# Optimization experiments

Hardware: AMD Instinct MI355X
Metric: run time of the kernel (lower is better)

The kernel has to match this reference:

```python
import jax, jax.numpy as jnp
import numpy as np

Q_MIN = 0.01
PT_THLD = 0.9
MAX_ETA = 4.0
LW_REP = 1.0
LW_NOISE = 0.1
LW_COWARD = 0.1
EPS = 1e-9

N_HITS = 50000
N_CLUSTERS = 1024  # cluster id 0 = noise, ids 1..K-1 = objects
D_EMB = 32


def setup_inputs() -> dict:
    key = jax.random.key(0)
    k0, k1, k2, k3, k4, k5 = jax.random.split(key, 6)
    beta = jax.random.uniform(k0, (N_HITS,), dtype=jnp.float32)
    x = jax.random.normal(k1, (N_HITS, D_EMB), dtype=jnp.float32)
    pt = jax.random.uniform(k2, (N_HITS,), dtype=jnp.float32)
    eta = jax.random.normal(k3, (N_HITS,), dtype=jnp.float32)
    reconstructable = jax.random.randint(k4, (N_HITS,), 0, 2, dtype=jnp.int32)
    cluster_ids = jax.random.randint(k5, (N_HITS,), 0, N_CLUSTERS, dtype=jnp.int64)
    return {
        'beta': beta, 'x': x, 'pt': pt, 'eta': eta,
        'reconstructable': reconstructable, 'cluster_ids': cluster_ids,
        'n_clusters': N_CLUSTERS,
    }


def reference(beta, x, pt, eta, reconstructable, cluster_ids, n_clusters):
    K = int(n_clusters)
    n_hits = beta.shape[0]
    n_part = K - 1  # objects of interest (excluding noise id 0)

    # charge q_j = arctanh(beta)^2 + q_min
    q = jnp.arctanh(jnp.clip(beta, 0.0, 1.0 - 1e-4)) ** 2 + Q_MIN  # [N]

    # attractive membership mask [N, K-1]: hit j belongs to object k and passes filters
    oids = jnp.arange(1, K)
    hit_ok = (reconstructable > 0) & (pt > PT_THLD) & (jnp.abs(eta) < MAX_ETA)
    att = (cluster_ids[:, None] == oids[None, :]) & hit_ok[:, None]
    attf = att.astype(q.dtype)

    # condensation point per object: hit with max charge within the object
    alphas = jnp.argmax(q[:, None] * attf, axis=0)  # [K-1]
    q_k = q[alphas]
    x_k = x[alphas]  # [K-1, D]

    # pairwise Euclidean distances, GEMM form (avoids [N,K,D] intermediate)
    d2 = (jnp.sum(x * x, axis=1)[:, None]
          + jnp.sum(x_k * x_k, axis=1)[None, :]
          - 2.0 * (x @ x_k.T))
    dist = jnp.sqrt(jnp.maximum(d2, 1e-12))  # [N, K-1]

    qw = q[:, None] * q_k[None, :]

    n_hits_oi = jnp.sum(hit_ok).astype(q.dtype)
    norm_att = EPS + n_hits_oi - n_part
    norm_rep = EPS + (n_part - 1) * n_hits

    v_att = jnp.sum(qw * (dist ** 2) * attf) / norm_att

    rep = (~att) & (dist < 1.0)  # max_n_rep=0 -> no subsampling
    v_rep = jnp.sum(qw * (1.0 - dist) * rep.astype(q.dtype)) / norm_rep

    l_coward = jnp.mean(1.0 - beta[alphas])

    noise_mask = (cluster_ids <= 0).astype(q.dtype)  # noise_threshold = 0
    l_noise = jnp.sum(beta * noise_mask) / jnp.maximum(jnp.sum(noise_mask), 1.0)

    total = v_att + LW_REP * v_rep + LW_NOISE * l_noise + LW_COWARD * l_coward
    return total
```

## Files before the change

### kernel.cpp

```cpp
#include <hip/hip_runtime.h>
#include <math.h>

namespace {

constexpr int D = 32;
constexpr int KOBJ = 1023;
constexpr float QMIN = 0.01f;
constexpr float PTT = 0.9f;
constexpr float METAETA = 4.0f;

typedef __attribute__((ext_vector_type(8))) short short8;
typedef __attribute__((ext_vector_type(4))) float f32x4;

#define GLOAD_LDS16(g, l)                                              \
  __builtin_amdgcn_global_load_lds(                                    \
      (const __attribute__((address_space(1))) void*)(g),              \
      (__attribute__((address_space(3))) void*)(l), 16, 0, 0)

__device__ inline float waveSum(float v) {
#pragma unroll
  for (int o = 32; o > 0; o >>= 1) v += __shfl_down(v, o, 64);
  return v;
}

__device__ inline ushort f2bf(float f) {
  unsigned u = __float_as_uint(f);
  return (ushort)((u + 0x7FFFu + ((u >> 16) & 1u)) >> 16);
}


__global__ __launch_bounds__(256) void k_hits(
    const float* __restrict__ beta, const float* __restrict__ x,
    const float* __restrict__ pt, const float* __restrict__ eta,
    const int* __restrict__ recon, const int* __restrict__ cidw,
    int N, float* acc, unsigned long long* keys,
    float* __restrict__ qArr, float* __restrict__ nxArr,
    int* __restrict__ attkArr) {
  int t = threadIdx.x;
  int j = blockIdx.x * 256 + t;
  int odd = 2 * (t & 127) + 1;
  int ow = (odd < N) ? cidw[odd] : 0;
  int is64 = !__any(ow != 0);
  bool ok = false;
  if (j < N) {
    int cid = is64 ? cidw[2 * j] : cidw[j];
    float b = beta[j];
    float bc = fminf(fmaxf(b, 0.f), 1.f - 1e-4f);
    float tt = atanhf(bc);
    float q = tt * tt + QMIN;
    ok = (recon[j] > 0) && (pt[j] > PTT) && (fabsf(eta[j]) < METAETA);
    float nx = 0.f;
    const float4* xr = (const float4*)(x + (size_t)j * D);
#pragma unroll
    for (int i2 = 0; i2 < 8; ++i2) {
      float4 v = xr[i2];
      nx += v.x * v.x + v.y * v.y + v.z * v.z + v.w * v.w;
    }
    int attk = (ok && cid >= 1) ? cid : 0;
    qArr[j] = q;
    nxArr[j] = nx;
    attkArr[j] = attk;
    if (cid <= 0) {
      atomicAdd(&acc[2], b);
      atomicAdd(&acc[3], 1.f);
    }
    if (attk >= 1) {
      unsigned long long key =
          (((unsigned long long)__float_as_uint(q)) << 32) |
          (unsigned long long)(0xFFFFFFFFu - (unsigned)j);
      atomicMax(&keys[attk - 1], key);
    }
  }
  unsigned long long bal = __ballot(ok);
  if ((t & 63) == 0 && bal)
    atomicAdd(&acc[4], (float)__popcll(bal));
}

__global__ __launch_bounds__(256, 2) void k_clusters(
    const float* __restrict__ beta, const float* __restrict__ x,
    const unsigned long long* __restrict__ keys,
    const float* __restrict__ qArr, const float* __restrict__ nxArr,
    int* __restrict__ alphaArr, float2* __restrict__ qnk,
    ushort* __restrict__ xkbT, float* acc) {
  int k = blockIdx.x * blockDim.x + threadIdx.x;
  float cw = 0.f;
  if (k < KOBJ) {
    unsigned long long key = keys[k];
    int alpha = (key != 0ull) ? (int)(0xFFFFFFFFu - (unsigned)(key & 0xFFFFFFFFull)) : 0;
    alphaArr[k] = alpha;
    qnk[k] = make_float2(qArr[alpha], nxArr[alpha]);
    const float4* s4 = (const float4*)(x + (size_t)alpha * D);
    float4 v[8];
#pragma unroll
    for (int i = 0; i < 8; ++i) v[i] = s4[i];
#pragma unroll
    for (int s = 0; s < 4; ++s) {
      float4 v0 = v[2 * s], v1 = v[2 * s + 1];
      ushort* dst = xkbT + (size_t)s * 8192 + (size_t)k * 8;
      dst[0] = f2bf(v0.x); dst[1] = f2bf(v0.y);
      dst[2] = f2bf(v0.z); dst[3] = f2bf(v0.w);
      dst[4] = f2bf(v1.x); dst[5] = f2bf(v1.y);
      dst[6] = f2bf(v1.z); dst[7] = f2bf(v1.w);
    }
    cw = 1.f - beta[alpha];
  } else if (k == KOBJ) {
    qnk[k] = make_float2(0.f, 1e30f);
#pragma unroll
    for (int s = 0; s < 4; ++s) {
      ushort* dst = xkbT + (size_t)s * 8192 + (size_t)k * 8;
#pragma unroll
      for (int e = 0; e < 8; ++e) dst[e] = 0;
    }
  }
  float s = waveSum(cw);
  if ((threadIdx.x & 63) == 0 && s != 0.f) atomicAdd(&acc[5], s);
}

__global__ __launch_bounds__(256) void k_pair(
    const float* __restrict__ x, int N,
    const float* __restrict__ qArr, const float* __restrict__ nxArr,
    const int* __restrict__ attkArr, const int* __restrict__ alphaArr,
    const float2* __restrict__ qnk, const ushort* __restrict__ xkbT,
    float* acc) {
  __shared__ char lds[16384 + 2048 + 64];
  float* redS = (float*)(lds + 18432);
  int t = threadIdx.x;
  int wv = t >> 6;
  int ln = t & 63;
  int ot = blockIdx.y;
  int ob = ot * 256;
  int rowbase = blockIdx.x * 128;

  for (int c = wv; c < 18; c += 4) {
    const char* src;
    if (c < 16)
      src = (const char*)xkbT + (c >> 2) * 16384 + ob * 16 + (c & 3) * 1024;
    else
      src = (const char*)qnk + ob * 8 + (c - 16) * 1024;
    GLOAD_LDS16(src + ln * 16, lds + c * 1024);
  }

  int lr = ln & 15;
  int lk = ln >> 4;
  int wrow = rowbase + wv * 32;

  short8 am2[2];
#pragma unroll
  for (int rt = 0; rt < 2; ++rt) {
    int row = min(wrow + rt * 16 + lr, N - 1);
    const float* p = x + (size_t)row * D + lk * 8;
    float4 v0 = *(const float4*)p;
    float4 v1 = *(const float4*)(p + 4);
    short8 a;
    a[0] = (short)f2bf(-2.f * v0.x); a[1] = (short)f2bf(-2.f * v0.y);
    a[2] = (short)f2bf(-2.f * v0.z); a[3] = (short)f2bf(-2.f * v0.w);
    a[4] = (short)f2bf(-2.f * v1.x); a[5] = (short)f2bf(-2.f * v1.y);
    a[6] = (short)f2bf(-2.f * v1.z); a[7] = (short)f2bf(-2.f * v1.w);
    am2[rt] = a;
  }
  float nxr[2][4], qrow[2][4];
#pragma unroll
  for (int rt = 0; rt < 2; ++rt)
#pragma unroll
    for (int i = 0; i < 4; ++i) {
      int row = wrow + rt * 16 + lk * 4 + i;
      int rc = min(row, N - 1);
      nxr[rt][i] = (row < N) ? nxArr[rc] : 1e37f;
      qrow[rt][i] = (row < N) ? qArr[rc] : 0.f;
    }
  __syncthreads();

  const float2* qnkS = (const float2*)(lds + 16384);
  float rep = 0.f;
#pragma unroll 4
  for (int tt = 0; tt < 16; ++tt) {
    int o = tt * 16 + lr;
    short8 b = *(const short8*)(lds + lk * 4096 + o * 16);
    float2 qn = qnkS[o];
    float nk = qn.y;
    f32x4 c0 = {nxr[0][0] + nk, nxr[0][1] + nk, nxr[0][2] + nk, nxr[0][3] + nk};
    f32x4 c1 = {nxr[1][0] + nk, nxr[1][1] + nk, nxr[1][2] + nk, nxr[1][3] + nk};
    f32x4 s0 = __builtin_amdgcn_mfma_f32_16x16x32_bf16(am2[0], b, c0, 0, 0, 0);
    f32x4 s1 = __builtin_amdgcn_mfma_f32_16x16x32_bf16(am2[1], b, c1, 0, 0, 0);
    float m = fminf(fminf(fminf(s0[0], s0[1]), fminf(s0[2], s0[3])),
                    fminf(fminf(s1[0], s1[1]), fminf(s1[2], s1[3])));
    if (__any(m < 1.f)) {
      float qk = qn.x;
#pragma unroll
      for (int i = 0; i < 4; ++i) {
        if (s0[i] < 1.f)
          rep += qrow[0][i] * qk * (1.f - sqrtf(fmaxf(s0[i], 1e-12f)));
        if (s1[i] < 1.f)
          rep += qrow[1][i] * qk * (1.f - sqrtf(fmaxf(s1[i], 1e-12f)));
      }
    }
  }

  float attc = 0.f, repSub = 0.f;
  if (ot == 0) {
    int j = rowbase + (t >> 1);
    int qt = t & 1;
    if (j < N) {
      int attk = attkArr[j];
      if (attk >= 1) {
        int k0 = attk - 1;
        int alpha = alphaArr[k0];
        float2 qn = qnk[k0];
        const float4* xj = (const float4*)(x + (size_t)j * D + qt * 16);
        const float4* xk = (const float4*)(x + (size_t)alpha * D + qt * 16);
        float dot = 0.f;
#pragma unroll
        for (int i = 0; i < 4; ++i) {
          float4 a = xj[i], bb = xk[i];
          dot += a.x * bb.x + a.y * bb.y + a.z * bb.z + a.w * bb.w;
        }
        dot += __shfl_xor(dot, 1, 2);
        if (qt == 0) {
          float d2 = nxArr[j] + qn.y - 2.f * dot;
          float w = qArr[j] * qn.x;
          attc = w * fmaxf(d2, 1e-12f);
          if (d2 < 1.f)
            repSub = w * (1.f - sqrtf(fmaxf(d2, 1e-12f)));
        }
      }
    }
  }

  float sw = waveSum(rep);
  float sa = waveSum(attc);
  float sr = waveSum(repSub);
  if (ln == 0) {
    redS[wv] = sw;
    redS[4 + wv] = sa;
    redS[8 + wv] = sr;
  }
  __syncthreads();
  if (t == 0) {
    float tot = (redS[0] + redS[1]) + (redS[2] + redS[3]);
    float ta = (redS[4] + redS[5]) + (redS[6] + redS[7]);
    float tr = (redS[8] + redS[9]) + (redS[10] + redS[11]);
    if (tot != tr) atomicAdd(&acc[1], tot - tr);
    if (ta != 0.f) atomicAdd(&acc[0], ta);
  }
}

__global__ void k_final(const float* __restrict__ acc, int N, float* out) {
  if (threadIdx.x == 0 && blockIdx.x == 0) {
    double attSum = acc[0], repSum = acc[1], noiseSum = acc[2];
    double noiseCnt = acc[3], okCnt = acc[4], cowardSum = acc[5];
    double norm_att = 1e-9 + okCnt - (double)KOBJ;
    double norm_rep = 1e-9 + (double)(KOBJ - 1) * (double)N;
    double v_att = attSum / norm_att;
    double v_rep = repSum / norm_rep;
    double l_coward = cowardSum / (double)KOBJ;
    double l_noise = noiseSum / fmax(noiseCnt, 1.0);
    out[0] = (float)(v_att + 1.0 * v_rep + 0.1 * l_noise + 0.1 * l_coward);
  }
}

}

extern "C" void kernel_launch(void* const* d_in, const int* in_sizes, int n_in,
                              void* d_out, int out_size, void* d_ws, size_t ws_size,
                              hipStream_t stream) {
  const float* beta = (const float*)d_in[0];
  const float* x = (const float*)d_in[1];
  const float* pt = (const float*)d_in[2];
  const float* eta = (const float*)d_in[3];
  const int* recon = (const int*)d_in[4];
  const int* cidw = (const int*)d_in[5];
  int N = in_sizes[0];
  float* out = (float*)d_out;

  char* w = (char*)d_ws;
  float* acc = (float*)w;
  unsigned long long* keys = (unsigned long long*)(w + 64);
  int* alphaArr = (int*)(w + 8256);
  float2* qnk = (float2*)(w + 12352);
  ushort* xkbT = (ushort*)(w + 20544);
  float* qArr = (float*)(w + 86080);
  float* nxArr = (float*)(w + 86080 + (size_t)N * 4);
  int* attkArr = (int*)(w + 86080 + (size_t)N * 8);

  int nbN = (N + 255) / 256;
  int rowgroups = (N + 127) / 128;

  hipMemsetAsync(w, 0, 8256, stream);
  k_hits<<<nbN, 256, 0, stream>>>(beta, x, pt, eta, recon, cidw, N,
                                  acc, keys, qArr, nxArr, attkArr);
  k_clusters<<<4, 256, 0, stream>>>(beta, x, keys, qArr, nxArr,
                                    alphaArr, qnk, xkbT, acc);
  dim3 gp(rowgroups, 4);
  k_pair<<<gp, 256, 0, stream>>>(x, N, qArr, nxArr, attkArr,
                                 alphaArr, qnk, xkbT, acc);
  k_final<<<1, 64, 0, stream>>>(acc, N, out);
}
```

Baseline: 53.58 us.

## Fuse cluster prep and final reduction into pair kernel, cut launches and atomics

```diff
diff --git a/kernel.cpp b/kernel.cpp
--- a/kernel.cpp
+++ b/kernel.cpp
@@ -12,11 +12,6 @@
 typedef __attribute__((ext_vector_type(8))) short short8;
 typedef __attribute__((ext_vector_type(4))) float f32x4;
 
-#define GLOAD_LDS16(g, l)                                              \
-  __builtin_amdgcn_global_load_lds(                                    \
-      (const __attribute__((address_space(1))) void*)(g),              \
-      (__attribute__((address_space(3))) void*)(l), 16, 0, 0)
-
 __device__ inline float waveSum(float v) {
 #pragma unroll
   for (int o = 32; o > 0; o >>= 1) v += __shfl_down(v, o, 64);
@@ -28,6 +23,13 @@
   return (ushort)((u + 0x7FFFu + ((u >> 16) & 1u)) >> 16);
 }
 
+__device__ inline int keyAlpha(unsigned long long key) {
+  return (key != 0ull) ? (int)(0xFFFFFFFFu - (unsigned)(key & 0xFFFFFFFFull)) : 0;
+}
+
+__global__ void k_init(int* wsbase) {
+  for (int k = threadIdx.x; k < 2064; k += 256) wsbase[k] = 0;
+}
 
 __global__ __launch_bounds__(256) void k_hits(
     const float* __restrict__ beta, const float* __restrict__ x,
@@ -42,6 +44,7 @@
   int ow = (odd < N) ? cidw[odd] : 0;
   int is64 = !__any(ow != 0);
   bool ok = false;
+  float nsum = 0.f, ncnt = 0.f;
   if (j < N) {
     int cid = is64 ? cidw[2 * j] : cidw[j];
     float b = beta[j];
@@ -60,10 +63,7 @@
     qArr[j] = q;
     nxArr[j] = nx;
     attkArr[j] = attk;
-    if (cid <= 0) {
-      atomicAdd(&acc[2], b);
-      atomicAdd(&acc[3], 1.f);
-    }
+    if (cid <= 0) { nsum = b; ncnt = 1.f; }
     if (attk >= 1) {
       unsigned long long key =
           (((unsigned long long)__float_as_uint(q)) << 32) |
@@ -71,59 +71,23 @@
       atomicMax(&keys[attk - 1], key);
     }
   }
+  float ws2 = waveSum(nsum);
+  float ws3 = waveSum(ncnt);
   unsigned long long bal = __ballot(ok);
-  if ((t & 63) == 0 && bal)
-    atomicAdd(&acc[4], (float)__popcll(bal));
-}
-
-__global__ __launch_bounds__(256, 2) void k_clusters(
-    const float* __restrict__ beta, const float* __restrict__ x,
-    const unsigned long long* __restrict__ keys,
+  if ((t & 63) == 0) {
+    if (ws3 != 0.f) { atomicAdd(&acc[2], ws2); atomicAdd(&acc[3], ws3); }
+    if (bal) atomicAdd(&acc[4], (float)__popcll(bal));
+  }
+}
+
+__global__ __launch_bounds__(256) void k_pair_all(
+    const float* __restrict__ beta, const float* __restrict__ x, int N,
     const float* __restrict__ qArr, const float* __restrict__ nxArr,
-    int* __restrict__ alphaArr, float2* __restrict__ qnk,
-    ushort* __restrict__ xkbT, float* acc) {
-  int k = blockIdx.x * blockDim.x + threadIdx.x;
-  float cw = 0.f;
-  if (k < KOBJ) {
-    unsigned long long key = keys[k];
-    int alpha = (key != 0ull) ? (int)(0xFFFFFFFFu - (unsigned)(key & 0xFFFFFFFFull)) : 0;
-    alphaArr[k] = alpha;
-    qnk[k] = make_float2(qArr[alpha], nxArr[alpha]);
-    const float4* s4 = (const float4*)(x + (size_t)alpha * D);
-    float4 v[8];
-#pragma unroll
-    for (int i = 0; i < 8; ++i) v[i] = s4[i];
-#pragma unroll
-    for (int s = 0; s < 4; ++s) {
-      float4 v0 = v[2 * s], v1 = v[2 * s + 1];
-      ushort* dst = xkbT + (size_t)s * 8192 + (size_t)k * 8;
-      dst[0] = f2bf(v0.x); dst[1] = f2bf(v0.y);
-      dst[2] = f2bf(v0.z); dst[3] = f2bf(v0.w);
-      dst[4] = f2bf(v1.x); dst[5] = f2bf(v1.y);
-      dst[6] = f2bf(v1.z); dst[7] = f2bf(v1.w);
-    }
-    cw = 1.f - beta[alpha];
-  } else if (k == KOBJ) {
-    qnk[k] = make_float2(0.f, 1e30f);
-#pragma unroll
-    for (int s = 0; s < 4; ++s) {
-      ushort* dst = xkbT + (size_t)s * 8192 + (size_t)k * 8;
-#pragma unroll
-      for (int e = 0; e < 8; ++e) dst[e] = 0;
-    }
-  }
-  float s = waveSum(cw);
-  if ((threadIdx.x & 63) == 0 && s != 0.f) atomicAdd(&acc[5], s);
-}
-
-__global__ __launch_bounds__(256) void k_pair(
-    const float* __restrict__ x, int N,
-    const float* __restrict__ qArr, const float* __restrict__ nxArr,
-    const int* __restrict__ attkArr, const int* __restrict__ alphaArr,
-    const float2* __restrict__ qnk, const ushort* __restrict__ xkbT,
-    float* acc) {
+    const int* __restrict__ attkArr, const unsigned long long* __restrict__ keys,
+    float* acc, unsigned* ticket, float* out) {
   __shared__ char lds[16384 + 2048 + 64];
   float* redS = (float*)(lds + 18432);
+  float2* qnkS = (float2*)(lds + 16384);
   int t = threadIdx.x;
   int wv = t >> 6;
   int ln = t & 63;
@@ -131,13 +95,39 @@
   int ob = ot * 256;
   int rowbase = blockIdx.x * 128;
 
-  for (int c = wv; c < 18; c += 4) {
-    const char* src;
-    if (c < 16)
-      src = (const char*)xkbT + (c >> 2) * 16384 + ob * 16 + (c & 3) * 1024;
-    else
-      src = (const char*)qnk + ob * 8 + (c - 16) * 1024;
-    GLOAD_LDS16(src + ln * 16, lds + c * 1024);
+  {
+    int o = ob + t;
+    float qk = 0.f, nk = 1e30f;
+    if (o < KOBJ) {
+      int alpha = keyAlpha(keys[o]);
+      qk = qArr[alpha];
+      nk = nxArr[alpha];
+      const float4* s4 = (const float4*)(x + (size_t)alpha * D);
+      float4 v[8];
+#pragma unroll
+      for (int i = 0; i < 8; ++i) v[i] = s4[i];
+#pragma unroll
+      for (int s = 0; s < 4; ++s) {
+        float4 v0 = v[2 * s], v1 = v[2 * s + 1];
+        short8 a;
+        a[0] = (short)f2bf(v0.x); a[1] = (short)f2bf(v0.y);
+        a[2] = (short)f2bf(v0.z); a[3] = (short)f2bf(v0.w);
+        a[4] = (short)f2bf(v1.x); a[5] = (short)f2bf(v1.y);
+        a[6] = (short)f2bf(v1.z); a[7] = (short)f2bf(v1.w);
+        *(short8*)(lds + s * 4096 + t * 16) = a;
+      }
+    } else {
+      short8 z = {0, 0, 0, 0, 0, 0, 0, 0};
+#pragma unroll
+      for (int s = 0; s < 4; ++s) *(short8*)(lds + s * 4096 + t * 16) = z;
+    }
+    qnkS[t] = make_float2(qk, nk);
+  }
+
+  float cw = 0.f;
+  if (blockIdx.x == 0) {
+    int o = ob + t;
+    if (o < KOBJ) cw = 1.f - beta[keyAlpha(keys[o])];
   }
 
   int lr = ln & 15;
@@ -170,7 +160,6 @@
     }
   __syncthreads();
 
-  const float2* qnkS = (const float2*)(lds + 16384);
   float rep = 0.f;
 #pragma unroll 4
   for (int tt = 0; tt < 16; ++tt) {
@@ -203,9 +192,7 @@
     if (j < N) {
       int attk = attkArr[j];
       if (attk >= 1) {
-        int k0 = attk - 1;
-        int alpha = alphaArr[k0];
-        float2 qn = qnk[k0];
+        int alpha = keyAlpha(keys[attk - 1]);
         const float4* xj = (const float4*)(x + (size_t)j * D + qt * 16);
         const float4* xk = (const float4*)(x + (size_t)alpha * D + qt * 16);
         float dot = 0.f;
@@ -216,8 +203,8 @@
         }
         dot += __shfl_xor(dot, 1, 2);
         if (qt == 0) {
-          float d2 = nxArr[j] + qn.y - 2.f * dot;
-          float w = qArr[j] * qn.x;
+          float d2 = nxArr[j] + nxArr[alpha] - 2.f * dot;
+          float w = qArr[j] * qArr[alpha];
           attc = w * fmaxf(d2, 1e-12f);
           if (d2 < 1.f)
             repSub = w * (1.f - sqrtf(fmaxf(d2, 1e-12f)));
@@ -229,32 +216,38 @@
   float sw = waveSum(rep);
   float sa = waveSum(attc);
   float sr = waveSum(repSub);
+  float sc = waveSum(cw);
   if (ln == 0) {
-    redS[wv] = sw;
-    redS[4 + wv] = sa;
-    redS[8 + wv] = sr;
+    redS[wv] = sw; redS[4 + wv] = sa; redS[8 + wv] = sr; redS[12 + wv] = sc;
   }
   __syncthreads();
   if (t == 0) {
     float tot = (redS[0] + redS[1]) + (redS[2] + redS[3]);
     float ta = (redS[4] + redS[5]) + (redS[6] + redS[7]);
     float tr = (redS[8] + redS[9]) + (redS[10] + redS[11]);
+    float tc = (redS[12] + redS[13]) + (redS[14] + redS[15]);
     if (tot != tr) atomicAdd(&acc[1], tot - tr);
     if (ta != 0.f) atomicAdd(&acc[0], ta);
-  }
-}
-
-__global__ void k_final(const float* __restrict__ acc, int N, float* out) {
-  if (threadIdx.x == 0 && blockIdx.x == 0) {
-    double attSum = acc[0], repSum = acc[1], noiseSum = acc[2];
-    double noiseCnt = acc[3], okCnt = acc[4], cowardSum = acc[5];
-    double norm_att = 1e-9 + okCnt - (double)KOBJ;
-    double norm_rep = 1e-9 + (double)(KOBJ - 1) * (double)N;
-    double v_att = attSum / norm_att;
-    double v_rep = repSum / norm_rep;
-    double l_coward = cowardSum / (double)KOBJ;
-    double l_noise = noiseSum / fmax(noiseCnt, 1.0);
-    out[0] = (float)(v_att + 1.0 * v_rep + 0.1 * l_noise + 0.1 * l_coward);
+    if (tc != 0.f) atomicAdd(&acc[5], tc);
+
+    unsigned total = gridDim.x * gridDim.y;
+    unsigned old = __hip_atomic_fetch_add(ticket, 1u, __ATOMIC_ACQ_REL,
+                                          __HIP_MEMORY_SCOPE_AGENT);
+    if (old == total - 1) {
+      double attSum = __hip_atomic_load(&acc[0], __ATOMIC_RELAXED, __HIP_MEMORY_SCOPE_AGENT);
+      double repSum = __hip_atomic_load(&acc[1], __ATOMIC_RELAXED, __HIP_MEMORY_SCOPE_AGENT);
+      double noiseSum = __hip_atomic_load(&acc[2], __ATOMIC_RELAXED, __HIP_MEMORY_SCOPE_AGENT);
+      double noiseCnt = __hip_atomic_load(&acc[3], __ATOMIC_RELAXED, __HIP_MEMORY_SCOPE_AGENT);
+      double okCnt = __hip_atomic_load(&acc[4], __ATOMIC_RELAXED, __HIP_MEMORY_SCOPE_AGENT);
+      double cowardSum = __hip_atomic_load(&acc[5], __ATOMIC_RELAXED, __HIP_MEMORY_SCOPE_AGENT);
+      double norm_att = 1e-9 + okCnt - (double)KOBJ;
+      double norm_rep = 1e-9 + (double)(KOBJ - 1) * (double)N;
+      double v_att = attSum / norm_att;
+      double v_rep = repSum / norm_rep;
+      double l_coward = cowardSum / (double)KOBJ;
+      double l_noise = noiseSum / fmax(noiseCnt, 1.0);
+      out[0] = (float)(v_att + 1.0 * v_rep + 0.1 * l_noise + 0.1 * l_coward);
+    }
   }
 }
 
@@ -274,10 +267,8 @@
 
   char* w = (char*)d_ws;
   float* acc = (float*)w;
+  unsigned* ticket = (unsigned*)(w + 32);
   unsigned long long* keys = (unsigned long long*)(w + 64);
-  int* alphaArr = (int*)(w + 8256);
-  float2* qnk = (float2*)(w + 12352);
-  ushort* xkbT = (ushort*)(w + 20544);
   float* qArr = (float*)(w + 86080);
   float* nxArr = (float*)(w + 86080 + (size_t)N * 4);
   int* attkArr = (int*)(w + 86080 + (size_t)N * 8);
@@ -285,13 +276,10 @@
   int nbN = (N + 255) / 256;
   int rowgroups = (N + 127) / 128;
 
-  hipMemsetAsync(w, 0, 8256, stream);
+  k_init<<<1, 256, 0, stream>>>((int*)w);
   k_hits<<<nbN, 256, 0, stream>>>(beta, x, pt, eta, recon, cidw, N,
                                   acc, keys, qArr, nxArr, attkArr);
-  k_clusters<<<4, 256, 0, stream>>>(beta, x, keys, qArr, nxArr,
-                                    alphaArr, qnk, xkbT, acc);
   dim3 gp(rowgroups, 4);
-  k_pair<<<gp, 256, 0, stream>>>(x, N, qArr, nxArr, attkArr,
-                                 alphaArr, qnk, xkbT, acc);
-  k_final<<<1, 64, 0, stream>>>(acc, N, out);
-}
+  k_pair_all<<<gp, 256, 0, stream>>>(beta, x, N, qArr, nxArr, attkArr,
+                                     keys, acc, ticket, out);
+}
```

Result: slower. 76.15 us (+42.1%).

## Fuse final reduction into pair kernel and load cluster tiles into registers

Applied to the files above, without the earlier changes.

```diff
diff --git a/kernel.cpp b/kernel.cpp
--- a/kernel.cpp
+++ b/kernel.cpp
@@ -12,11 +12,6 @@
 typedef __attribute__((ext_vector_type(8))) short short8;
 typedef __attribute__((ext_vector_type(4))) float f32x4;
 
-#define GLOAD_LDS16(g, l)                                              \
-  __builtin_amdgcn_global_load_lds(                                    \
-      (const __attribute__((address_space(1))) void*)(g),              \
-      (__attribute__((address_space(3))) void*)(l), 16, 0, 0)
-
 __device__ inline float waveSum(float v) {
 #pragma unroll
   for (int o = 32; o > 0; o >>= 1) v += __shfl_down(v, o, 64);
@@ -28,6 +23,13 @@
   return (ushort)((u + 0x7FFFu + ((u >> 16) & 1u)) >> 16);
 }
 
+__device__ inline int keyAlpha(unsigned long long key) {
+  return (key != 0ull) ? (int)(0xFFFFFFFFu - (unsigned)(key & 0xFFFFFFFFull)) : 0;
+}
+
+__global__ void k_init(int* wsbase) {
+  for (int k = threadIdx.x; k < 2064; k += 256) wsbase[k] = 0;
+}
 
 __global__ __launch_bounds__(256) void k_hits(
     const float* __restrict__ beta, const float* __restrict__ x,
@@ -42,6 +44,7 @@
   int ow = (odd < N) ? cidw[odd] : 0;
   int is64 = !__any(ow != 0);
   bool ok = false;
+  float nsum = 0.f, ncnt = 0.f;
   if (j < N) {
     int cid = is64 ? cidw[2 * j] : cidw[j];
     float b = beta[j];
@@ -60,10 +63,7 @@
     qArr[j] = q;
     nxArr[j] = nx;
     attkArr[j] = attk;
-    if (cid <= 0) {
-      atomicAdd(&acc[2], b);
-      atomicAdd(&acc[3], 1.f);
-    }
+    if (cid <= 0) { nsum = b; ncnt = 1.f; }
     if (attk >= 1) {
       unsigned long long key =
           (((unsigned long long)__float_as_uint(q)) << 32) |
@@ -71,9 +71,13 @@
       atomicMax(&keys[attk - 1], key);
     }
   }
+  float ws2 = waveSum(nsum);
+  float ws3 = waveSum(ncnt);
   unsigned long long bal = __ballot(ok);
-  if ((t & 63) == 0 && bal)
-    atomicAdd(&acc[4], (float)__popcll(bal));
+  if ((t & 63) == 0) {
+    if (ws3 != 0.f) { atomicAdd(&acc[2], ws2); atomicAdd(&acc[3], ws3); }
+    if (bal) atomicAdd(&acc[4], (float)__popcll(bal));
+  }
 }
 
 __global__ __launch_bounds__(256, 2) void k_clusters(
@@ -85,8 +89,7 @@
   int k = blockIdx.x * blockDim.x + threadIdx.x;
   float cw = 0.f;
   if (k < KOBJ) {
-    unsigned long long key = keys[k];
-    int alpha = (key != 0ull) ? (int)(0xFFFFFFFFu - (unsigned)(key & 0xFFFFFFFFull)) : 0;
+    int alpha = keyAlpha(keys[k]);
     alphaArr[k] = alpha;
     qnk[k] = make_float2(qArr[alpha], nxArr[alpha]);
     const float4* s4 = (const float4*)(x + (size_t)alpha * D);
@@ -116,32 +119,20 @@
   if ((threadIdx.x & 63) == 0 && s != 0.f) atomicAdd(&acc[5], s);
 }
 
-__global__ __launch_bounds__(256) void k_pair(
-    const float* __restrict__ x, int N,
+__global__ __launch_bounds__(256, 2) void k_pair(
+    const float* __restrict__ beta, const float* __restrict__ x, int N,
     const float* __restrict__ qArr, const float* __restrict__ nxArr,
     const int* __restrict__ attkArr, const int* __restrict__ alphaArr,
     const float2* __restrict__ qnk, const ushort* __restrict__ xkbT,
-    float* acc) {
-  __shared__ char lds[16384 + 2048 + 64];
-  float* redS = (float*)(lds + 18432);
+    float* acc, unsigned* ticket, float* out) {
+  __shared__ float redS[16];
   int t = threadIdx.x;
   int wv = t >> 6;
   int ln = t & 63;
-  int ot = blockIdx.y;
-  int ob = ot * 256;
-  int rowbase = blockIdx.x * 128;
-
-  for (int c = wv; c < 18; c += 4) {
-    const char* src;
-    if (c < 16)
-      src = (const char*)xkbT + (c >> 2) * 16384 + ob * 16 + (c & 3) * 1024;
-    else
-      src = (const char*)qnk + ob * 8 + (c - 16) * 1024;
-    GLOAD_LDS16(src + ln * 16, lds + c * 1024);
-  }
-
   int lr = ln & 15;
   int lk = ln >> 4;
+  int ob = blockIdx.y * 256;
+  int rowbase = blockIdx.x * 128;
   int wrow = rowbase + wv * 32;
 
   short8 am2[2];
@@ -168,36 +159,43 @@
       nxr[rt][i] = (row < N) ? nxArr[rc] : 1e37f;
       qrow[rt][i] = (row < N) ? qArr[rc] : 0.f;
     }
-  __syncthreads();
-
-  const float2* qnkS = (const float2*)(lds + 16384);
+
+  const char* xb = (const char*)xkbT + lk * 16384 + (size_t)(ob + lr) * 16;
+  const float2* qb = qnk + ob + lr;
+  short8 B0, B1, B2, B3, B4, B5, B6, B7, B8, B9, B10, B11, B12, B13, B14, B15;
+  float2 Q0, Q1, Q2, Q3, Q4, Q5, Q6, Q7, Q8, Q9, Q10, Q11, Q12, Q13, Q14, Q15;
+#define LD(i) B##i = *(const short8*)(xb + (i) * 256); Q##i = qb[(i) * 16];
+  LD(0) LD(1) LD(2) LD(3) LD(4) LD(5) LD(6) LD(7)
+  LD(8) LD(9) LD(10) LD(11) LD(12) LD(13) LD(14) LD(15)
+#undef LD
+
   float rep = 0.f;
-#pragma unroll 4
-  for (int tt = 0; tt < 16; ++tt) {
-    int o = tt * 16 + lr;
-    short8 b = *(const short8*)(lds + lk * 4096 + o * 16);
-    float2 qn = qnkS[o];
-    float nk = qn.y;
-    f32x4 c0 = {nxr[0][0] + nk, nxr[0][1] + nk, nxr[0][2] + nk, nxr[0][3] + nk};
-    f32x4 c1 = {nxr[1][0] + nk, nxr[1][1] + nk, nxr[1][2] + nk, nxr[1][3] + nk};
-    f32x4 s0 = __builtin_amdgcn_mfma_f32_16x16x32_bf16(am2[0], b, c0, 0, 0, 0);
-    f32x4 s1 = __builtin_amdgcn_mfma_f32_16x16x32_bf16(am2[1], b, c1, 0, 0, 0);
-    float m = fminf(fminf(fminf(s0[0], s0[1]), fminf(s0[2], s0[3])),
-                    fminf(fminf(s1[0], s1[1]), fminf(s1[2], s1[3])));
-    if (__any(m < 1.f)) {
-      float qk = qn.x;
-#pragma unroll
-      for (int i = 0; i < 4; ++i) {
-        if (s0[i] < 1.f)
-          rep += qrow[0][i] * qk * (1.f - sqrtf(fmaxf(s0[i], 1e-12f)));
-        if (s1[i] < 1.f)
-          rep += qrow[1][i] * qk * (1.f - sqrtf(fmaxf(s1[i], 1e-12f)));
-      }
-    }
-  }
+#define STEP(i)                                                                \
+  {                                                                            \
+    float nk = Q##i.y;                                                         \
+    f32x4 c0 = {nxr[0][0] + nk, nxr[0][1] + nk, nxr[0][2] + nk, nxr[0][3] + nk}; \
+    f32x4 c1 = {nxr[1][0] + nk, nxr[1][1] + nk, nxr[1][2] + nk, nxr[1][3] + nk}; \
+    f32x4 s0 = __builtin_amdgcn_mfma_f32_16x16x32_bf16(am2[0], B##i, c0, 0, 0, 0); \
+    f32x4 s1 = __builtin_amdgcn_mfma_f32_16x16x32_bf16(am2[1], B##i, c1, 0, 0, 0); \
+    float m = fminf(fminf(fminf(s0[0], s0[1]), fminf(s0[2], s0[3])),           \
+                    fminf(fminf(s1[0], s1[1]), fminf(s1[2], s1[3])));          \
+    if (__any(m < 1.f)) {                                                      \
+      float qk = Q##i.x;                                                       \
+      _Pragma("unroll")                                                        \
+      for (int ii = 0; ii < 4; ++ii) {                                         \
+        if (s0[ii] < 1.f)                                                      \
+          rep += qrow[0][ii] * qk * (1.f - sqrtf(fmaxf(s0[ii], 1e-12f)));      \
+        if (s1[ii] < 1.f)                                                      \
+          rep += qrow[1][ii] * qk * (1.f - sqrtf(fmaxf(s1[ii], 1e-12f)));      \
+      }                                                                        \
+    }                                                                          \
+  }
+  STEP(0) STEP(1) STEP(2) STEP(3) STEP(4) STEP(5) STEP(6) STEP(7)
+  STEP(8) STEP(9) STEP(10) STEP(11) STEP(12) STEP(13) STEP(14) STEP(15)
+#undef STEP
 
   float attc = 0.f, repSub = 0.f;
-  if (ot == 0) {
+  if (blockIdx.y == 0) {
     int j = rowbase + (t >> 1);
     int qt = t & 1;
     if (j < N) {
@@ -229,11 +227,7 @@
   float sw = waveSum(rep);
   float sa = waveSum(attc);
   float sr = waveSum(repSub);
-  if (ln == 0) {
-    redS[wv] = sw;
-    redS[4 + wv] = sa;
-    redS[8 + wv] = sr;
-  }
+  if (ln == 0) { redS[wv] = sw; redS[4 + wv] = sa; redS[8 + wv] = sr; }
   __syncthreads();
   if (t == 0) {
     float tot = (redS[0] + redS[1]) + (redS[2] + redS[3]);
@@ -241,20 +235,25 @@
     float tr = (redS[8] + redS[9]) + (redS[10] + redS[11]);
     if (tot != tr) atomicAdd(&acc[1], tot - tr);
     if (ta != 0.f) atomicAdd(&acc[0], ta);
-  }
-}
-
-__global__ void k_final(const float* __restrict__ acc, int N, float* out) {
-  if (threadIdx.x == 0 && blockIdx.x == 0) {
-    double attSum = acc[0], repSum = acc[1], noiseSum = acc[2];
-    double noiseCnt = acc[3], okCnt = acc[4], cowardSum = acc[5];
-    double norm_att = 1e-9 + okCnt - (double)KOBJ;
-    double norm_rep = 1e-9 + (double)(KOBJ - 1) * (double)N;
-    double v_att = attSum / norm_att;
-    double v_rep = repSum / norm_rep;
-    double l_coward = cowardSum / (double)KOBJ;
-    double l_noise = noiseSum / fmax(noiseCnt, 1.0);
-    out[0] = (float)(v_att + 1.0 * v_rep + 0.1 * l_noise + 0.1 * l_coward);
+
+    unsigned total = gridDim.x * gridDim.y;
+    unsigned old = __hip_atomic_fetch_add(ticket, 1u, __ATOMIC_ACQ_REL,
+                                          __HIP_MEMORY_SCOPE_AGENT);
+    if (old == total - 1) {
+      double attSum = __hip_atomic_load(&acc[0], __ATOMIC_RELAXED, __HIP_MEMORY_SCOPE_AGENT);
+      double repSum = __hip_atomic_load(&acc[1], __ATOMIC_RELAXED, __HIP_MEMORY_SCOPE_AGENT);
+      double noiseSum = __hip_atomic_load(&acc[2], __ATOMIC_RELAXED, __HIP_MEMORY_SCOPE_AGENT);
+      double noiseCnt = __hip_atomic_load(&acc[3], __ATOMIC_RELAXED, __HIP_MEMORY_SCOPE_AGENT);
+      double okCnt = __hip_atomic_load(&acc[4], __ATOMIC_RELAXED, __HIP_MEMORY_SCOPE_AGENT);
+      double cowardSum = __hip_atomic_load(&acc[5], __ATOMIC_RELAXED, __HIP_MEMORY_SCOPE_AGENT);
+      double norm_att = 1e-9 + okCnt - (double)KOBJ;
+      double norm_rep = 1e-9 + (double)(KOBJ - 1) * (double)N;
+      double v_att = attSum / norm_att;
+      double v_rep = repSum / norm_rep;
+      double l_coward = cowardSum / (double)KOBJ;
+      double l_noise = noiseSum / fmax(noiseCnt, 1.0);
+      out[0] = (float)(v_att + 1.0 * v_rep + 0.1 * l_noise + 0.1 * l_coward);
+    }
   }
 }
 
@@ -274,6 +273,7 @@
 
   char* w = (char*)d_ws;
   float* acc = (float*)w;
+  unsigned* ticket = (unsigned*)(w + 32);
   unsigned long long* keys = (unsigned long long*)(w + 64);
   int* alphaArr = (int*)(w + 8256);
   float2* qnk = (float2*)(w + 12352);
@@ -285,13 +285,12 @@
   int nbN = (N + 255) / 256;
   int rowgroups = (N + 127) / 128;
 
-  hipMemsetAsync(w, 0, 8256, stream);
+  k_init<<<1, 256, 0, stream>>>((int*)w);
   k_hits<<<nbN, 256, 0, stream>>>(beta, x, pt, eta, recon, cidw, N,
                                   acc, keys, qArr, nxArr, attkArr);
   k_clusters<<<4, 256, 0, stream>>>(beta, x, keys, qArr, nxArr,
                                     alphaArr, qnk, xkbT, acc);
   dim3 gp(rowgroups, 4);
-  k_pair<<<gp, 256, 0, stream>>>(x, N, qArr, nxArr, attkArr,
-                                 alphaArr, qnk, xkbT, acc);
-  k_final<<<1, 64, 0, stream>>>(acc, N, out);
-}
+  k_pair<<<gp, 256, 0, stream>>>(beta, x, N, qArr, nxArr, attkArr,
+                                 alphaArr, qnk, xkbT, acc, ticket, out);
+}
```

Result: slower. 77.30 us (+44.3%).

## Fold final reduction into pair kernel, replace memset with init kernel, wave-reduce noise atomics

Applied to the files above, without the earlier changes.

```diff
diff --git a/kernel.cpp b/kernel.cpp
--- a/kernel.cpp
+++ b/kernel.cpp
@@ -28,6 +28,13 @@
   return (ushort)((u + 0x7FFFu + ((u >> 16) & 1u)) >> 16);
 }
 
+__device__ inline int keyAlpha(unsigned long long key) {
+  return (key != 0ull) ? (int)(0xFFFFFFFFu - (unsigned)(key & 0xFFFFFFFFull)) : 0;
+}
+
+__global__ void k_init(int* wsbase) {
+  for (int k = threadIdx.x; k < 2064; k += 256) wsbase[k] = 0;
+}
 
 __global__ __launch_bounds__(256) void k_hits(
     const float* __restrict__ beta, const float* __restrict__ x,
@@ -42,6 +49,7 @@
   int ow = (odd < N) ? cidw[odd] : 0;
   int is64 = !__any(ow != 0);
   bool ok = false;
+  float nsum = 0.f, ncnt = 0.f;
   if (j < N) {
     int cid = is64 ? cidw[2 * j] : cidw[j];
     float b = beta[j];
@@ -60,10 +68,7 @@
     qArr[j] = q;
     nxArr[j] = nx;
     attkArr[j] = attk;
-    if (cid <= 0) {
-      atomicAdd(&acc[2], b);
-      atomicAdd(&acc[3], 1.f);
-    }
+    if (cid <= 0) { nsum = b; ncnt = 1.f; }
     if (attk >= 1) {
       unsigned long long key =
           (((unsigned long long)__float_as_uint(q)) << 32) |
@@ -71,9 +76,13 @@
       atomicMax(&keys[attk - 1], key);
     }
   }
+  float ws2 = waveSum(nsum);
+  float ws3 = waveSum(ncnt);
   unsigned long long bal = __ballot(ok);
-  if ((t & 63) == 0 && bal)
-    atomicAdd(&acc[4], (float)__popcll(bal));
+  if ((t & 63) == 0) {
+    if (ws3 != 0.f) { atomicAdd(&acc[2], ws2); atomicAdd(&acc[3], ws3); }
+    if (bal) atomicAdd(&acc[4], (float)__popcll(bal));
+  }
 }
 
 __global__ __launch_bounds__(256, 2) void k_clusters(
@@ -85,8 +94,7 @@
   int k = blockIdx.x * blockDim.x + threadIdx.x;
   float cw = 0.f;
   if (k < KOBJ) {
-    unsigned long long key = keys[k];
-    int alpha = (key != 0ull) ? (int)(0xFFFFFFFFu - (unsigned)(key & 0xFFFFFFFFull)) : 0;
+    int alpha = keyAlpha(keys[k]);
     alphaArr[k] = alpha;
     qnk[k] = make_float2(qArr[alpha], nxArr[alpha]);
     const float4* s4 = (const float4*)(x + (size_t)alpha * D);
@@ -121,7 +129,7 @@
     const float* __restrict__ qArr, const float* __restrict__ nxArr,
     const int* __restrict__ attkArr, const int* __restrict__ alphaArr,
     const float2* __restrict__ qnk, const ushort* __restrict__ xkbT,
-    float* acc) {
+    float* acc, unsigned* ticket, float* out) {
   __shared__ char lds[16384 + 2048 + 64];
   float* redS = (float*)(lds + 18432);
   int t = threadIdx.x;
@@ -229,11 +237,7 @@
   float sw = waveSum(rep);
   float sa = waveSum(attc);
   float sr = waveSum(repSub);
-  if (ln == 0) {
-    redS[wv] = sw;
-    redS[4 + wv] = sa;
-    redS[8 + wv] = sr;
-  }
+  if (ln == 0) { redS[wv] = sw; redS[4 + wv] = sa; redS[8 + wv] = sr; }
   __syncthreads();
   if (t == 0) {
     float tot = (redS[0] + redS[1]) + (redS[2] + redS[3]);
@@ -241,20 +245,25 @@
     float tr = (redS[8] + redS[9]) + (redS[10] + redS[11]);
     if (tot != tr) atomicAdd(&acc[1], tot - tr);
     if (ta != 0.f) atomicAdd(&acc[0], ta);
-  }
-}
-
-__global__ void k_final(const float* __restrict__ acc, int N, float* out) {
-  if (threadIdx.x == 0 && blockIdx.x == 0) {
-    double attSum = acc[0], repSum = acc[1], noiseSum = acc[2];
-    double noiseCnt = acc[3], okCnt = acc[4], cowardSum = acc[5];
-    double norm_att = 1e-9 + okCnt - (double)KOBJ;
-    double norm_rep = 1e-9 + (double)(KOBJ - 1) * (double)N;
-    double v_att = attSum / norm_att;
-    double v_rep = repSum / norm_rep;
-    double l_coward = cowardSum / (double)KOBJ;
-    double l_noise = noiseSum / fmax(noiseCnt, 1.0);
-    out[0] = (float)(v_att + 1.0 * v_rep + 0.1 * l_noise + 0.1 * l_coward);
+
+    unsigned total = gridDim.x * gridDim.y;
+    unsigned old = __hip_atomic_fetch_add(ticket, 1u, __ATOMIC_ACQ_REL,
+                                          __HIP_MEMORY_SCOPE_AGENT);
+    if (old == total - 1) {
+      double attSum = __hip_atomic_load(&acc[0], __ATOMIC_RELAXED, __HIP_MEMORY_SCOPE_AGENT);
+      double repSum = __hip_atomic_load(&acc[1], __ATOMIC_RELAXED, __HIP_MEMORY_SCOPE_AGENT);
+      double noiseSum = __hip_atomic_load(&acc[2], __ATOMIC_RELAXED, __HIP_MEMORY_SCOPE_AGENT);
+      double noiseCnt = __hip_atomic_load(&acc[3], __ATOMIC_RELAXED, __HIP_MEMORY_SCOPE_AGENT);
+      double okCnt = __hip_atomic_load(&acc[4], __ATOMIC_RELAXED, __HIP_MEMORY_SCOPE_AGENT);
+      double cowardSum = __hip_atomic_load(&acc[5], __ATOMIC_RELAXED, __HIP_MEMORY_SCOPE_AGENT);
+      double norm_att = 1e-9 + okCnt - (double)KOBJ;
+      double norm_rep = 1e-9 + (double)(KOBJ - 1) * (double)N;
+      double v_att = attSum / norm_att;
+      double v_rep = repSum / norm_rep;
+      double l_coward = cowardSum / (double)KOBJ;
+      double l_noise = noiseSum / fmax(noiseCnt, 1.0);
+      out[0] = (float)(v_att + 1.0 * v_rep + 0.1 * l_noise + 0.1 * l_coward);
+    }
   }
 }
 
@@ -274,6 +283,7 @@
 
   char* w = (char*)d_ws;
   float* acc = (float*)w;
+  unsigned* ticket = (unsigned*)(w + 32);
   unsigned long long* keys = (unsigned long long*)(w + 64);
   int* alphaArr = (int*)(w + 8256);
   float2* qnk = (float2*)(w + 12352);
@@ -285,13 +295,12 @@
   int nbN = (N + 255) / 256;
   int rowgroups = (N + 127) / 128;
 
-  hipMemsetAsync(w, 0, 8256, stream);
+  k_init<<<1, 256, 0, stream>>>((int*)w);
   k_hits<<<nbN, 256, 0, stream>>>(beta, x, pt, eta, recon, cidw, N,
                                   acc, keys, qArr, nxArr, attkArr);
   k_clusters<<<4, 256, 0, stream>>>(beta, x, keys, qArr, nxArr,
                                     alphaArr, qnk, xkbT, acc);
   dim3 gp(rowgroups, 4);
   k_pair<<<gp, 256, 0, stream>>>(x, N, qArr, nxArr, attkArr,
-                                 alphaArr, qnk, xkbT, acc);
-  k_final<<<1, 64, 0, stream>>>(acc, N, out);
-}
+                                 alphaArr, qnk, xkbT, acc, ticket, out);
+}
```

Result: slower. 75.70 us (+41.3%).
